# Kernel optimization log

Hardware: AMD Instinct MI355X
Metric: run time of the kernel (lower is better)

Reference implementation:

```python
import jax, jax.numpy as jnp
import numpy as np
from jax import lax

B, IN_N, MID_N, OUT_N, K, L, WH = 16, 256, 256, 256, 3, 4096, 1024
EPS = 1e-5


def att_conv(x, W, b=None):
    # x: [B, Cin, L], W: [B, Cout, Cin, K] -> per-sample conv1d, padding='same'
    pl, pr = (K - 1) // 2, K // 2
    xp = jnp.pad(x, ((0, 0), (0, 0), (pl, pr)))
    out = 0.
    for t in range(K):  # small fixed K, unrolled shifted-slice einsum
        out = out + jnp.einsum('bcl,boc->bol', lax.dynamic_slice_in_dim(xp, t, L, 2), W[..., t])
    if b is not None:
        out = out + b[:, :, None]
    return out


def batch_norm(x, w, b):
    # training-mode BN over (N, L) per channel, biased variance
    mean = x.mean((0, 2), keepdims=True)
    var = ((x - mean) ** 2).mean((0, 2), keepdims=True)
    return (x - mean) * (w[None, :, None] / jnp.sqrt(var + EPS)) + b[None, :, None]


def se_module(x, w1, b1, w2, b2):
    s = x.mean(2, keepdims=True)  # [B, C, 1]
    s = jax.nn.relu(jnp.einsum('bcl,oc->bol', s, w1) + b1[None, :, None])
    s = jax.nn.sigmoid(jnp.einsum('bcl,oc->bol', s, w2) + b2[None, :, None])
    return x * s


def setup_inputs() -> dict:
    key = jax.random.key(0)
    ks = jax.random.split(key, 16)
    f = lambda k, sh, sc=0.02: jax.random.normal(k, sh, jnp.float32) * sc
    return {
        'x': f(ks[0], (B, IN_N, L), 1.0),
        'att1': f(ks[1], (B, MID_N, WH), 1.0),
        'att2': f(ks[2], (B, MID_N, WH), 1.0),
        'att3': f(ks[3], (B, OUT_N, WH), 1.0),
        'w1_w': f(ks[4], (IN_N * K, WH)), 'w1_b': jnp.zeros((IN_N * K,), jnp.float32),
        'w2_w': f(ks[5], (MID_N * K, WH)), 'w2_b': jnp.zeros((MID_N * K,), jnp.float32),
        'w3_w': f(ks[6], (MID_N * K, WH)), 'w3_b': jnp.zeros((MID_N * K,), jnp.float32),
        'b1_w': f(ks[7], (1, WH)), 'b1_b': jnp.zeros((1,), jnp.float32),
        'bn2_w': jnp.full((MID_N,), 0.1, jnp.float32), 'bn2_b': jnp.zeros((MID_N,), jnp.float32),
        'bn3_w': jnp.full((OUT_N,), 0.1, jnp.float32), 'bn3_b': jnp.zeros((OUT_N,), jnp.float32),
        'se1_w': f(ks[8], (OUT_N, OUT_N)), 'se1_b': jnp.zeros((OUT_N,), jnp.float32),
        'se2_w': f(ks[9], (OUT_N, OUT_N)), 'se2_b': jnp.zeros((OUT_N,), jnp.float32),
    }


def reference(x, att1, att2, att3, w1_w, w1_b, w2_w, w2_b, w3_w, w3_b,
              b1_w, b1_b, bn2_w, bn2_b, bn3_w, bn3_b, se1_w, se1_b, se2_w, se2_b):
    shortcut = x  # in_n == out_n, no downsample -> Identity
    # hypernetwork weight generation (Linear on last dim)
    W1 = (att1 @ w1_w.T + w1_b).reshape(B, MID_N, IN_N, K)
    W2 = (att2 @ w2_w.T + w2_b).reshape(B, MID_N, MID_N, K)
    W3 = (att3 @ w3_w.T + w3_b).reshape(B, OUT_N, MID_N, K)
    b1 = (att1 @ b1_w.T + b1_b)[..., 0]  # [B, mid_n]
    h = jax.nn.relu(att_conv(x, W1, b1))
    h = jax.nn.relu(batch_norm(att_conv(h, W2), bn2_w, bn2_b))
    h = jax.nn.relu(batch_norm(att_conv(h, W3), bn3_w, bn3_b))
    out = jax.nn.relu(se_module(h, se1_w, se1_b, se2_w, se2_b) + shortcut)
    return out
```

## Files before the change

### kernel.cpp

```cpp
#include <hip/hip_runtime.h>
#include <hip/hip_bf16.h>

using bf16 = __hip_bfloat16;
typedef __attribute__((ext_vector_type(4))) float f32x4;
typedef __attribute__((ext_vector_type(8))) short short8;
typedef __attribute__((ext_vector_type(2))) unsigned int uint2v;
typedef __attribute__((ext_vector_type(4))) unsigned int uint4v;

#define DEVI static __device__ __forceinline__

DEVI unsigned short f2b(float f){
  unsigned int u = __float_as_uint(f);
  unsigned int r = (u + 0x7fffu + ((u >> 16) & 1u)) >> 16;
  return (unsigned short)r;
}
DEVI float b2f(unsigned short u){
  return __uint_as_float(((unsigned int)u) << 16);
}

DEVI void gload16(const void* g, void* l){
  __builtin_amdgcn_global_load_lds(
      (const __attribute__((address_space(1))) unsigned int*)g,
      (__attribute__((address_space(3))) unsigned int*)l, 16, 0, 0);
}

__global__ __launch_bounds__(256) void k_transpose_x(const float* __restrict__ x,
                                                     bf16* __restrict__ xt)
{
  __shared__ float tile[64][65];
  const int b = blockIdx.z, l0 = blockIdx.x*64, c0 = blockIdx.y*64;
  const int tid = threadIdx.x;
  {
    const int r = tid >> 2, q = tid & 3;
    const float* src = x + ((size_t)(b*256 + c0 + r))*4096 + l0 + q*16;
    #pragma unroll
    for (int j = 0; j < 4; ++j){
      const f32x4 v = *reinterpret_cast<const f32x4*>(src + j*4);
      #pragma unroll
      for (int e = 0; e < 4; ++e) tile[r][q*16 + j*4 + e] = v[e];
    }
  }
  __syncthreads();
  {
    const int jr = tid >> 2, cq = tid & 3;
    unsigned int w[8];
    #pragma unroll
    for (int e = 0; e < 8; ++e){
      const float lo = tile[cq*16 + 2*e][jr];
      const float hi = tile[cq*16 + 2*e + 1][jr];
      w[e] = (unsigned int)f2b(lo) | ((unsigned int)f2b(hi) << 16);
    }
    unsigned short* dst = (unsigned short*)xt + ((size_t)b*4098 + l0 + jr + 1)*256 + c0 + cq*16;
    uint4v a0 = {w[0],w[1],w[2],w[3]}, a1 = {w[4],w[5],w[6],w[7]};
    *reinterpret_cast<uint4v*>(dst)     = a0;
    *reinterpret_cast<uint4v*>(dst + 8) = a1;
  }
}

__global__ void k_zero_pads(bf16* __restrict__ xt, bf16* __restrict__ h1t)
{
  const int b = blockIdx.x, tid = threadIdx.x;
  const size_t top = (size_t)b*4098*256 + tid;
  const size_t bot = (size_t)b*4098*256 + (size_t)4097*256 + tid;
  unsigned short* px = (unsigned short*)xt;
  unsigned short* ph = (unsigned short*)h1t;
  px[top] = 0; px[bot] = 0; ph[top] = 0; ph[bot] = 0;
}

__global__ __launch_bounds__(256) void k_cvt3(const float* __restrict__ s0, const float* __restrict__ s1,
                                              const float* __restrict__ s2, bf16* __restrict__ dst, int n1)
{
  const size_t total = (size_t)3 * (size_t)n1 / 4;
  for (size_t i = (size_t)blockIdx.x*256 + threadIdx.x; i < total; i += (size_t)gridDim.x*256){
    const size_t e = i*4;
    const int which = (int)(e / (size_t)n1);
    const size_t off = e - (size_t)which*(size_t)n1;
    const float* s = which==0 ? s0 : which==1 ? s1 : s2;
    const f32x4 v = *reinterpret_cast<const f32x4*>(s + off);
    uint2v p;
    p[0] = (unsigned)f2b(v[0]) | ((unsigned)f2b(v[1])<<16);
    p[1] = (unsigned)f2b(v[2]) | ((unsigned)f2b(v[3])<<16);
    *reinterpret_cast<uint2v*>((unsigned short*)dst + e) = p;
  }
}


__global__ __launch_bounds__(512, 2) void k_gen(const bf16* __restrict__ attb, const bf16* __restrict__ wbp,
                                                const float* __restrict__ bias0, const float* __restrict__ bias1,
                                                const float* __restrict__ bias2, bf16* __restrict__ Wt)
{
  __shared__ bf16 sAll[4*16384];
  const int flat = blockIdx.x + (blockIdx.z << 4);
  const int xcd = flat & 7, s = flat >> 3;
  const int t = s % 3, tau = (s/3)*8 + xcd;
  const int i = tau >> 4, bo = tau & 15;
  const int bo0 = bo*256;
  const bf16* __restrict__ A  = wbp  + (size_t)i*768*1024 + (size_t)t*1024;
  const bf16* __restrict__ Bt = attb + (size_t)i*4096*1024 + (size_t)bo0*1024;
  const float* __restrict__ bias = (i==0) ? bias0 : (i==1) ? bias1 : bias2;
  const int tid = threadIdx.x, lane = tid & 63, wid = tid >> 6;
  const int wr = wid >> 2, wc = wid & 3;
  const int frow = lane & 15, g = lane >> 4;
  f32x4 acc[8][4] = {};

#define GEN_STAGE(kt, bufi) { \
    const int kc = (kt)*64; \
    _Pragma("unroll") \
    for (int j = 0; j < 4; ++j){ \
      const int slot = tid + j*512, r = slot >> 3, s7 = slot & 7; \
      const int cc = (s7 ^ (r & 7)) * 8; \
      gload16(A + (size_t)r*3072 + kc + cc, &sAll[(bufi)*16384 + slot*8]); \
    } \
    _Pragma("unroll") \
    for (int j = 0; j < 4; ++j){ \
      const int slot = tid + j*512, r = slot >> 3, s7 = slot & 7; \
      const int cc = (s7 ^ (r & 7)) * 8; \
      gload16(Bt + (size_t)r*1024 + kc + cc, &sAll[32768 + (bufi)*16384 + slot*8]); \
    } \
  }

  GEN_STAGE(0, 0);
  #pragma unroll 1
  for (int kt = 0; kt < 16; ++kt){
    const int buf = kt & 1;
    if (kt + 1 < 16){
      GEN_STAGE(kt+1, buf^1);
      asm volatile("s_waitcnt vmcnt(8)" ::: "memory");
    } else {
      asm volatile("s_waitcnt vmcnt(0)" ::: "memory");
    }
    __builtin_amdgcn_s_barrier();
    __builtin_amdgcn_sched_barrier(0);
    const bf16* pA = sAll + buf*16384;
    const bf16* pB = sAll + 32768 + buf*16384;
    #pragma unroll
    for (int ks = 0; ks < 2; ++ks){
      short8 bfr[4];
      #pragma unroll
      for (int n = 0; n < 4; ++n){
        const int row = wc*64 + n*16 + frow;
        const int sl = (ks*4 + g) ^ (row & 7);
        bfr[n] = *reinterpret_cast<const short8*>(pB + row*64 + sl*8);
      }
      __builtin_amdgcn_s_setprio(1);
      #pragma unroll
      for (int m = 0; m < 8; ++m){
        const int row = wr*128 + m*16 + frow;
        const int sl = (ks*4 + g) ^ (row & 7);
        const short8 af = *reinterpret_cast<const short8*>(pA + row*64 + sl*8);
        #pragma unroll
        for (int n = 0; n < 4; ++n)
          acc[m][n] = __builtin_amdgcn_mfma_f32_16x16x32_bf16(af, bfr[n], acc[m][n], 0, 0, 0);
      }
      __builtin_amdgcn_s_setprio(0);
    }
    __builtin_amdgcn_sched_barrier(0);
    __builtin_amdgcn_s_barrier();
    __builtin_amdgcn_sched_barrier(0);
  }
#undef GEN_STAGE

  #pragma unroll
  for (int m = 0; m < 8; ++m){
    const int col = wr*128 + m*16 + g*4;
    float bi[4];
    #pragma unroll
    for (int j = 0; j < 4; ++j) bi[j] = bias[(col + j)*3 + t];
    #pragma unroll
    for (int n = 0; n < 4; ++n){
      const int row = wc*64 + n*16 + frow;
      uint2v p;
      p[0] = (unsigned)f2b(acc[m][n][0] + bi[0]) | ((unsigned)f2b(acc[m][n][1] + bi[1]) << 16);
      p[1] = (unsigned)f2b(acc[m][n][2] + bi[2]) | ((unsigned)f2b(acc[m][n][3] + bi[3]) << 16);
      const int chunk = (col >> 3) ^ (row & 31);
      *reinterpret_cast<uint2v*>((char*)sAll + row*512 + chunk*16 + (g&1)*8) = p;
    }
  }
  __syncthreads();
  {
    char* gp = (char*)Wt + 2*(((size_t)(i*16 + bo)*3 + t)*65536);
    #pragma unroll
    for (int p2 = 0; p2 < 16; ++p2){
      const int row = p2*16 + (tid >> 5);
      const int c = tid & 31;
      const int cs2 = c ^ (row & 31);
      const uint4v v = *reinterpret_cast<const uint4v*>((const char*)sAll + row*512 + cs2*16);
      *reinterpret_cast<uint4v*>(gp + (size_t)row*512 + c*16) = v;
    }
  }
}

__global__ __launch_bounds__(256) void k_b1(const float* __restrict__ att1, const float* __restrict__ b1w,
                                            const float* __restrict__ b1b, float* __restrict__ out)
{
  const int m = blockIdx.x*4 + (threadIdx.x >> 6);
  const int lane = threadIdx.x & 63;
  const float* a = att1 + (size_t)m*1024;
  float s = 0.f;
  for (int k = lane*4; k < 1024; k += 256){
    const f32x4 v = *reinterpret_cast<const f32x4*>(a + k);
    const f32x4 w = *reinterpret_cast<const f32x4*>(b1w + k);
    s += v[0]*w[0] + v[1]*w[1] + v[2]*w[2] + v[3]*w[3];
  }
  #pragma unroll
  for (int d = 32; d > 0; d >>= 1) s += __shfl_down(s, d);
  if (lane == 0) out[m] = s + b1b[0];
}

__global__ __launch_bounds__(512, 2) void k_conv(const bf16* __restrict__ Xt, const bf16* __restrict__ W,
                                                 const float* __restrict__ bias, bf16* __restrict__ out,
                                                 int outBatchStride, int outRowOff, int applyRelu,
                                                 float* __restrict__ statSum, float* __restrict__ statSq)
{
  __shared__ bf16 sAll[4*16384];
  const int flat = blockIdx.x + (blockIdx.z << 4);
  const int xcd = flat & 7, slot = flat >> 3;
  const int b = 2*xcd + (slot >> 4);
  const int l0 = (slot & 15)*256;
  const int tid = threadIdx.x, lane = tid & 63, wid = tid >> 6;
  const int wr = wid >> 2, wc = wid & 3;
  const int frow = lane & 15, g = lane >> 4;
  f32x4 acc[8][4] = {};

#define CONV_STAGE(kt, bufi) { \
    const int ct3 = (kt)/3, tt = (kt) - ct3*3, c0 = ct3*64; \
    const bf16* Ab = W  + (((size_t)b*3 + tt)*256)*256 + c0; \
    const bf16* Bb = Xt + ((size_t)b*4098 + l0 + tt)*256 + c0; \
    _Pragma("unroll") \
    for (int j = 0; j < 4; ++j){ \
      const int slotq = tid + j*512, r = slotq >> 3, s7 = slotq & 7; \
      const int cc = (s7 ^ (r & 7)) * 8; \
      gload16(Ab + (size_t)r*256 + cc, &sAll[(bufi)*16384 + slotq*8]); \
    } \
    _Pragma("unroll") \
    for (int j = 0; j < 4; ++j){ \
      const int slotq = tid + j*512, r = slotq >> 3, s7 = slotq & 7; \
      const int cc = (s7 ^ (r & 7)) * 8; \
      gload16(Bb + (size_t)r*256 + cc, &sAll[32768 + (bufi)*16384 + slotq*8]); \
    } \
  }

  CONV_STAGE(0, 0);
  #pragma unroll 1
  for (int kt = 0; kt < 12; ++kt){
    const int buf = kt & 1;
    if (kt + 1 < 12){
      CONV_STAGE(kt+1, buf^1);
      asm volatile("s_waitcnt vmcnt(8)" ::: "memory");
    } else {
      asm volatile("s_waitcnt vmcnt(0)" ::: "memory");
    }
    __builtin_amdgcn_s_barrier();
    __builtin_amdgcn_sched_barrier(0);
    const bf16* pA = sAll + buf*16384;
    const bf16* pB = sAll + 32768 + buf*16384;
    #pragma unroll
    for (int ks = 0; ks < 2; ++ks){
      short8 bfr[4];
      #pragma unroll
      for (int n = 0; n < 4; ++n){
        const int row = wc*64 + n*16 + frow;
        const int sl = (ks*4 + g) ^ (row & 7);
        bfr[n] = *reinterpret_cast<const short8*>(pB + row*64 + sl*8);
      }
      __builtin_amdgcn_s_setprio(1);
      #pragma unroll
      for (int m = 0; m < 8; ++m){
        const int row = wr*128 + m*16 + frow;
        const int sl = (ks*4 + g) ^ (row & 7);
        const short8 af = *reinterpret_cast<const short8*>(pA + row*64 + sl*8);
        #pragma unroll
        for (int n = 0; n < 4; ++n)
          acc[m][n] = __builtin_amdgcn_mfma_f32_16x16x32_bf16(af, bfr[n], acc[m][n], 0, 0, 0);
      }
      __builtin_amdgcn_s_setprio(0);
    }
    __builtin_amdgcn_sched_barrier(0);
    __builtin_amdgcn_s_barrier();
    __builtin_amdgcn_sched_barrier(0);
  }
#undef CONV_STAGE

  float cs[8][4] = {{0.f}}, cq[8][4] = {{0.f}};
  #pragma unroll
  for (int m = 0; m < 8; ++m){
    const int col = wr*128 + m*16 + g*4;
    float bi[4] = {0.f, 0.f, 0.f, 0.f};
    if (bias){
      const f32x4 bv = *reinterpret_cast<const f32x4*>(bias + b*256 + col);
      bi[0]=bv[0]; bi[1]=bv[1]; bi[2]=bv[2]; bi[3]=bv[3];
    }
    #pragma unroll
    for (int n = 0; n < 4; ++n){
      const int row = wc*64 + n*16 + frow;
      float v[4];
      #pragma unroll
      for (int j = 0; j < 4; ++j){
        v[j] = acc[m][n][j] + bi[j];
        if (applyRelu) v[j] = fmaxf(v[j], 0.f);
        cs[m][j] += v[j];
        cq[m][j] += v[j]*v[j];
      }
      uint2v p;
      p[0] = (unsigned)f2b(v[0]) | ((unsigned)f2b(v[1]) << 16);
      p[1] = (unsigned)f2b(v[2]) | ((unsigned)f2b(v[3]) << 16);
      const int chunk = (col >> 3) ^ (row & 31);
      *reinterpret_cast<uint2v*>((char*)sAll + row*512 + chunk*16 + (g&1)*8) = p;
    }
  }
  __syncthreads();
  {
    char* gp = (char*)out + 2*((size_t)b*outBatchStride + (size_t)(l0 + outRowOff)*256);
    #pragma unroll
    for (int p2 = 0; p2 < 16; ++p2){
      const int row = p2*16 + (tid >> 5);
      const int c = tid & 31;
      const int cs2 = c ^ (row & 31);
      const uint4v v = *reinterpret_cast<const uint4v*>((const char*)sAll + row*512 + cs2*16);
      *reinterpret_cast<uint4v*>(gp + (size_t)row*512 + c*16) = v;
    }
  }
  if (statSum){
    #pragma unroll
    for (int m = 0; m < 8; ++m)
      #pragma unroll
      for (int j = 0; j < 4; ++j){
        #pragma unroll
        for (int d = 1; d < 16; d <<= 1){
          cs[m][j] += __shfl_xor(cs[m][j], d);
          cq[m][j] += __shfl_xor(cq[m][j], d);
        }
      }
    __syncthreads();
    float* ls = (float*)sAll;
    float* lq = ls + 1024;
    if (frow == 0){
      #pragma unroll
      for (int m = 0; m < 8; ++m)
        #pragma unroll
        for (int j = 0; j < 4; ++j){
          ls[wid*128 + m*16 + g*4 + j] = cs[m][j];
          lq[wid*128 + m*16 + g*4 + j] = cq[m][j];
        }
    }
    __syncthreads();
    if (tid < 256){
      const int o = tid, half = o >> 7, idx = o & 127;
      float s = 0.f, qq = 0.f;
      #pragma unroll
      for (int wv = 0; wv < 4; ++wv){
        s  += ls[(half*4 + wv)*128 + idx];
        qq += lq[(half*4 + wv)*128 + idx];
      }
      atomicAdd(statSum + o, s);
      atomicAdd(statSq  + o, qq);
    }
  }
}

__global__ void k_bnfin(const float* __restrict__ sum, const float* __restrict__ sq,
                        const float* __restrict__ g, const float* __restrict__ bb,
                        float* __restrict__ scale, float* __restrict__ shift)
{
  const int o = threadIdx.x;
  const float inv = 1.f/65536.f;
  const float m = sum[o]*inv;
  const float v = fmaxf(sq[o]*inv - m*m, 0.f);
  const float sc = g[o] / sqrtf(v + 1e-5f);
  scale[o] = sc;
  shift[o] = bb[o] - m*sc;
}

__global__ __launch_bounds__(256) void k_norm2(const bf16* __restrict__ y, const float* __restrict__ scale,
                                               const float* __restrict__ shift, bf16* __restrict__ h)
{
  const int gr = blockIdx.x*8 + (threadIdx.x >> 5);
  const int oc = threadIdx.x & 31;
  const int b = gr / 4098, lp = gr - b*4098;
  unsigned short* dst = (unsigned short*)h + (size_t)gr*256 + oc*8;
  if (lp == 0 || lp == 4097){
    uint4v z = {0u,0u,0u,0u};
    *reinterpret_cast<uint4v*>(dst) = z;
    return;
  }
  const unsigned short* src = (const unsigned short*)y + ((size_t)b*4096 + (lp-1))*256 + oc*8;
  const uint4v in = *reinterpret_cast<const uint4v*>(src);
  const f32x4 sA0 = *reinterpret_cast<const f32x4*>(scale + oc*8);
  const f32x4 sA1 = *reinterpret_cast<const f32x4*>(scale + oc*8 + 4);
  const f32x4 hA0 = *reinterpret_cast<const f32x4*>(shift + oc*8);
  const f32x4 hA1 = *reinterpret_cast<const f32x4*>(shift + oc*8 + 4);
  uint4v ov;
  #pragma unroll
  for (int e = 0; e < 4; ++e){
    const unsigned int w = in[e];
    const float sc0 = (e<2) ? sA0[2*e] : sA1[2*e-4];
    const float sc1 = (e<2) ? sA0[2*e+1] : sA1[2*e-3];
    const float sh0 = (e<2) ? hA0[2*e] : hA1[2*e-4];
    const float sh1 = (e<2) ? hA0[2*e+1] : hA1[2*e-3];
    const float v0 = fmaxf(b2f((unsigned short)(w & 0xffffu))*sc0 + sh0, 0.f);
    const float v1 = fmaxf(b2f((unsigned short)(w >> 16))*sc1 + sh1, 0.f);
    ov[e] = (unsigned)f2b(v0) | ((unsigned)f2b(v1) << 16);
  }
  *reinterpret_cast<uint4v*>(dst) = ov;
}

__global__ __launch_bounds__(256) void k_norm3(bf16* __restrict__ y, const float* __restrict__ scale,
                                               const float* __restrict__ shift, float* __restrict__ s_sum)
{
  __shared__ float red[8][256];
  const int tid = threadIdx.x;
  const int rr = tid >> 5, oc = tid & 31;
  const size_t row = (size_t)blockIdx.x*8 + rr;
  const int b = (int)(row >> 12);
  unsigned short* p = (unsigned short*)y + row*256 + oc*8;
  const uint4v in = *reinterpret_cast<const uint4v*>(p);
  const f32x4 sA0 = *reinterpret_cast<const f32x4*>(scale + oc*8);
  const f32x4 sA1 = *reinterpret_cast<const f32x4*>(scale + oc*8 + 4);
  const f32x4 hA0 = *reinterpret_cast<const f32x4*>(shift + oc*8);
  const f32x4 hA1 = *reinterpret_cast<const f32x4*>(shift + oc*8 + 4);
  uint4v ov;
  float loc[8];
  #pragma unroll
  for (int e = 0; e < 4; ++e){
    const unsigned int w = in[e];
    const float sc0 = (e<2) ? sA0[2*e] : sA1[2*e-4];
    const float sc1 = (e<2) ? sA0[2*e+1] : sA1[2*e-3];
    const float sh0 = (e<2) ? hA0[2*e] : hA1[2*e-4];
    const float sh1 = (e<2) ? hA0[2*e+1] : hA1[2*e-3];
    const float v0 = fmaxf(b2f((unsigned short)(w & 0xffffu))*sc0 + sh0, 0.f);
    const float v1 = fmaxf(b2f((unsigned short)(w >> 16))*sc1 + sh1, 0.f);
    loc[2*e] = v0; loc[2*e+1] = v1;
    ov[e] = (unsigned)f2b(v0) | ((unsigned)f2b(v1) << 16);
  }
  *reinterpret_cast<uint4v*>(p) = ov;
  #pragma unroll
  for (int j = 0; j < 8; ++j) red[rr][oc*8 + j] = loc[j];
  __syncthreads();
  const int o = tid;
  float tot = 0.f;
  #pragma unroll
  for (int r2 = 0; r2 < 8; ++r2) tot += red[r2][o];
  atomicAdd(&s_sum[(size_t)b*256 + o], tot);
}

__global__ __launch_bounds__(256) void k_se(const float* __restrict__ s_sum, const float* __restrict__ w1,
                                            const float* __restrict__ b1, const float* __restrict__ w2,
                                            const float* __restrict__ b2, float* __restrict__ s2)
{
  __shared__ float sv[256];
  __shared__ float t1[256];
  const int b = blockIdx.x, o = threadIdx.x;
  sv[o] = s_sum[(size_t)b*256 + o] * (1.f/4096.f);
  __syncthreads();
  float a = b1[o];
  for (int c = 0; c < 256; ++c) a += w1[(size_t)o*256 + c] * sv[c];
  t1[o] = fmaxf(a, 0.f);
  __syncthreads();
  float a2 = b2[o];
  for (int c = 0; c < 256; ++c) a2 += w2[(size_t)o*256 + c] * t1[c];
  s2[(size_t)b*256 + o] = 1.f / (1.f + expf(-a2));
}

__global__ __launch_bounds__(256) void k_final(const bf16* __restrict__ h3, const float* __restrict__ s2,
                                               const float* __restrict__ x, float* __restrict__ out)
{
  __shared__ float tile[64][65];
  const int b = blockIdx.z, o0 = blockIdx.y*64, l0 = blockIdx.x*64;
  const int tid = threadIdx.x;
  {
    const int r = tid >> 2, q = tid & 3;
    const unsigned short* src = (const unsigned short*)h3 + ((size_t)b*4096 + l0 + r)*256 + o0 + q*16;
    const uint4v a0 = *reinterpret_cast<const uint4v*>(src);
    const uint4v a1 = *reinterpret_cast<const uint4v*>(src + 8);
    #pragma unroll
    for (int e = 0; e < 4; ++e){
      tile[r][q*16 + 2*e]         = b2f((unsigned short)(a0[e] & 0xffffu));
      tile[r][q*16 + 2*e + 1]     = b2f((unsigned short)(a0[e] >> 16));
      tile[r][q*16 + 8 + 2*e]     = b2f((unsigned short)(a1[e] & 0xffffu));
      tile[r][q*16 + 8 + 2*e + 1] = b2f((unsigned short)(a1[e] >> 16));
    }
  }
  __syncthreads();
  {
    const int orow = tid >> 2, q = tid & 3;
    const int o = o0 + orow;
    const float sc = s2[(size_t)b*256 + o];
    const float* xs = x + ((size_t)b*256 + o)*4096 + l0 + q*16;
    float* dst = out + ((size_t)b*256 + o)*4096 + l0 + q*16;
    #pragma unroll
    for (int k = 0; k < 16; k += 4){
      const f32x4 xv = *reinterpret_cast<const f32x4*>(xs + k);
      f32x4 r;
      #pragma unroll
      for (int e = 0; e < 4; ++e)
        r[e] = fmaxf(tile[q*16 + k + e][orow]*sc + xv[e], 0.f);
      *reinterpret_cast<f32x4*>(dst + k) = r;
    }
  }
}

extern "C" void kernel_launch(void* const* d_in, const int* in_sizes, int n_in,
                              void* d_out, int out_size, void* d_ws, size_t ws_size,
                              hipStream_t stream)
{
  const float* x     = (const float*)d_in[0];
  const float* att1  = (const float*)d_in[1];
  const float* att2  = (const float*)d_in[2];
  const float* att3  = (const float*)d_in[3];
  const float* w1_w  = (const float*)d_in[4];
  const float* w1_b  = (const float*)d_in[5];
  const float* w2_w  = (const float*)d_in[6];
  const float* w2_b  = (const float*)d_in[7];
  const float* w3_w  = (const float*)d_in[8];
  const float* w3_b  = (const float*)d_in[9];
  const float* b1_w  = (const float*)d_in[10];
  const float* b1_b  = (const float*)d_in[11];
  const float* bn2_w = (const float*)d_in[12];
  const float* bn2_b = (const float*)d_in[13];
  const float* bn3_w = (const float*)d_in[14];
  const float* bn3_b = (const float*)d_in[15];
  const float* se1_w = (const float*)d_in[16];
  const float* se1_b = (const float*)d_in[17];
  const float* se2_w = (const float*)d_in[18];
  const float* se2_b = (const float*)d_in[19];

  char* ws = (char*)d_ws;
  bf16*  xT   = (bf16*)(ws + 0);
  bf16*  h1T  = (bf16*)(ws + 33570816);
  bf16*  y2T  = (bf16*)(ws + 67141632);
  bf16*  h2T  = (bf16*)(ws + 100696064);
  bf16*  Wt   = (bf16*)(ws + 134266880);
  bf16*  attb = (bf16*)(ws + 153141248);
  bf16*  wb   = (bf16*)(ws + 178307072);
  float* b1v  = (float*)(ws + 183025664);
  float* st   = (float*)(ws + 183042048);
  float* bn2sum = st;
  float* bn2sq  = st + 256;
  float* bn3sum = st + 512;
  float* bn3sq  = st + 768;
  float* s_sum  = st + 1024;
  float* scale2 = st + 5120;
  float* shift2 = st + 5376;
  float* scale3 = st + 5632;
  float* shift3 = st + 5888;
  float* s2v    = st + 6144;
  bf16*  y3T  = (bf16*)(ws + 0);

  hipMemsetAsync(st, 0, 5120*sizeof(float), stream);

  k_transpose_x<<<dim3(64,4,16),256,0,stream>>>(x, xT);
  k_zero_pads<<<16,256,0,stream>>>(xT, h1T);
  k_cvt3<<<2048,256,0,stream>>>(att1, att2, att3, attb, 4096*1024);
  k_cvt3<<<512,256,0,stream>>>(w1_w, w2_w, w3_w, wb, 768*1024);
  k_gen<<<dim3(16,1,9),512,0,stream>>>(attb, wb, w1_b, w2_b, w3_b, Wt);
  k_b1<<<1024,256,0,stream>>>(att1, b1_w, b1_b, b1v);

  k_conv<<<dim3(16,1,16),512,0,stream>>>(xT,  Wt,                           b1v,     h1T, 4098*256, 1, 1, nullptr, nullptr);
  k_conv<<<dim3(16,1,16),512,0,stream>>>(h1T, Wt + (size_t)1*16*3*256*256,  nullptr, y2T, 4096*256, 0, 0, bn2sum, bn2sq);
  k_bnfin<<<1,256,0,stream>>>(bn2sum, bn2sq, bn2_w, bn2_b, scale2, shift2);
  k_norm2<<<8196,256,0,stream>>>(y2T, scale2, shift2, h2T);
  k_conv<<<dim3(16,1,16),512,0,stream>>>(h2T, Wt + (size_t)2*16*3*256*256,  nullptr, y3T, 4096*256, 0, 0, bn3sum, bn3sq);
  k_bnfin<<<1,256,0,stream>>>(bn3sum, bn3sq, bn3_w, bn3_b, scale3, shift3);
  k_norm3<<<8192,256,0,stream>>>(y3T, scale3, shift3, s_sum);
  k_se<<<16,256,0,stream>>>(s_sum, se1_w, se1_b, se2_w, se2_b, s2v);
  k_final<<<dim3(64,4,16),256,0,stream>>>((const bf16*)y3T, s2v, x, (float*)d_out);
}
```

Measured before the change: 309.2 us.

## Fuse att fp32-to-bf16 conversion into hypernet GEMM and shrink conv tiles

The hypernetwork GEMM now loads fp32 attention rows straight from global memory into registers, converts them to bf16 and writes them to LDS itself. This removes the separate conversion kernel and its bf16 round trip through memory. The K step is halved to 32 to fit the smaller LDS budget, and the epilogue is split into two passes. The conv kernel now uses 256x128 tiles with a K step of 32, twice as many blocks and launch bounds of 4 blocks per CU, to raise occupancy. The trade is more barriers per unit of K and less reuse per tile.

```diff
diff --git a/kernel.cpp b/kernel.cpp
--- a/kernel.cpp
+++ b/kernel.cpp
@@ -84,109 +84,134 @@
   }
 }
 
-
-__global__ __launch_bounds__(512, 2) void k_gen(const bf16* __restrict__ attb, const bf16* __restrict__ wbp,
+__global__ __launch_bounds__(512, 2) void k_gen(const float* __restrict__ att1f, const float* __restrict__ att2f,
+                                                const float* __restrict__ att3f, const bf16* __restrict__ wbp,
                                                 const float* __restrict__ bias0, const float* __restrict__ bias1,
                                                 const float* __restrict__ bias2, bf16* __restrict__ Wt)
 {
-  __shared__ bf16 sAll[4*16384];
+  __shared__ bf16 sAll[32768];
   const int flat = blockIdx.x + (blockIdx.z << 4);
   const int xcd = flat & 7, s = flat >> 3;
   const int t = s % 3, tau = (s/3)*8 + xcd;
   const int i = tau >> 4, bo = tau & 15;
   const int bo0 = bo*256;
-  const bf16* __restrict__ A  = wbp  + (size_t)i*768*1024 + (size_t)t*1024;
-  const bf16* __restrict__ Bt = attb + (size_t)i*4096*1024 + (size_t)bo0*1024;
+  const bf16*  __restrict__ A  = wbp + (size_t)i*768*1024 + (size_t)t*1024;
+  const float* __restrict__ Bf = ((i==0) ? att1f : (i==1) ? att2f : att3f) + (size_t)bo0*1024;
   const float* __restrict__ bias = (i==0) ? bias0 : (i==1) ? bias1 : bias2;
   const int tid = threadIdx.x, lane = tid & 63, wid = tid >> 6;
   const int wr = wid >> 2, wc = wid & 3;
   const int frow = lane & 15, g = lane >> 4;
   f32x4 acc[8][4] = {};
-
-#define GEN_STAGE(kt, bufi) { \
-    const int kc = (kt)*64; \
+  f32x4 rN[4];
+
+  const int rB = tid >> 1, hB = tid & 1;
+  const float* bsBase = Bf + (size_t)rB*1024 + hB*16;
+
+#define GEN_STAGE_A(kt, bufi) { \
     _Pragma("unroll") \
-    for (int j = 0; j < 4; ++j){ \
-      const int slot = tid + j*512, r = slot >> 3, s7 = slot & 7; \
-      const int cc = (s7 ^ (r & 7)) * 8; \
-      gload16(A + (size_t)r*3072 + kc + cc, &sAll[(bufi)*16384 + slot*8]); \
-    } \
-    _Pragma("unroll") \
-    for (int j = 0; j < 4; ++j){ \
-      const int slot = tid + j*512, r = slot >> 3, s7 = slot & 7; \
-      const int cc = (s7 ^ (r & 7)) * 8; \
-      gload16(Bt + (size_t)r*1024 + kc + cc, &sAll[32768 + (bufi)*16384 + slot*8]); \
-    } \
-  }
-
-  GEN_STAGE(0, 0);
+    for (int j = 0; j < 2; ++j){ \
+      const int q = tid + j*512, r = q >> 2, s3 = q & 3; \
+      const int cc = (s3 ^ ((r >> 1) & 3)) * 8; \
+      gload16(A + (size_t)r*3072 + (kt)*32 + cc, &sAll[(bufi)*8192 + q*8]); \
+    } }
+
+#define GEN_WRITE_B(bufi) { \
+    unsigned short* wp = (unsigned short*)&sAll[16384 + (bufi)*8192]; \
+    uint4v w0, w1; \
+    w0[0] = (unsigned)f2b(rN[0][0]) | ((unsigned)f2b(rN[0][1])<<16); \
+    w0[1] = (unsigned)f2b(rN[0][2]) | ((unsigned)f2b(rN[0][3])<<16); \
+    w0[2] = (unsigned)f2b(rN[1][0]) | ((unsigned)f2b(rN[1][1])<<16); \
+    w0[3] = (unsigned)f2b(rN[1][2]) | ((unsigned)f2b(rN[1][3])<<16); \
+    w1[0] = (unsigned)f2b(rN[2][0]) | ((unsigned)f2b(rN[2][1])<<16); \
+    w1[1] = (unsigned)f2b(rN[2][2]) | ((unsigned)f2b(rN[2][3])<<16); \
+    w1[2] = (unsigned)f2b(rN[3][0]) | ((unsigned)f2b(rN[3][1])<<16); \
+    w1[3] = (unsigned)f2b(rN[3][2]) | ((unsigned)f2b(rN[3][3])<<16); \
+    const int sl0 = (hB*2 + 0) ^ ((rB >> 1) & 3); \
+    const int sl1 = (hB*2 + 1) ^ ((rB >> 1) & 3); \
+    *reinterpret_cast<uint4v*>(wp + rB*32 + sl0*8) = w0; \
+    *reinterpret_cast<uint4v*>(wp + rB*32 + sl1*8) = w1; }
+
+  #pragma unroll
+  for (int q = 0; q < 4; ++q) rN[q] = *reinterpret_cast<const f32x4*>(bsBase + q*4);
+  GEN_STAGE_A(0, 0);
+  asm volatile("s_waitcnt vmcnt(0)" ::: "memory");
+  GEN_WRITE_B(0);
+  asm volatile("s_waitcnt lgkmcnt(0)" ::: "memory");
+  __builtin_amdgcn_s_barrier();
+
   #pragma unroll 1
-  for (int kt = 0; kt < 16; ++kt){
-    const int buf = kt & 1;
-    if (kt + 1 < 16){
-      GEN_STAGE(kt+1, buf^1);
-      asm volatile("s_waitcnt vmcnt(8)" ::: "memory");
+  for (int kt = 0; kt < 32; ++kt){
+    const int p = kt & 1;
+    if (kt + 1 < 32){
+      #pragma unroll
+      for (int q = 0; q < 4; ++q) rN[q] = *reinterpret_cast<const f32x4*>(bsBase + (kt+1)*32 + q*4);
+      GEN_STAGE_A(kt+1, p^1);
+      asm volatile("s_waitcnt vmcnt(6)" ::: "memory");
     } else {
       asm volatile("s_waitcnt vmcnt(0)" ::: "memory");
     }
     __builtin_amdgcn_s_barrier();
-    __builtin_amdgcn_sched_barrier(0);
-    const bf16* pA = sAll + buf*16384;
-    const bf16* pB = sAll + 32768 + buf*16384;
-    #pragma unroll
-    for (int ks = 0; ks < 2; ++ks){
-      short8 bfr[4];
-      #pragma unroll
-      for (int n = 0; n < 4; ++n){
-        const int row = wc*64 + n*16 + frow;
-        const int sl = (ks*4 + g) ^ (row & 7);
-        bfr[n] = *reinterpret_cast<const short8*>(pB + row*64 + sl*8);
-      }
-      __builtin_amdgcn_s_setprio(1);
-      #pragma unroll
-      for (int m = 0; m < 8; ++m){
-        const int row = wr*128 + m*16 + frow;
-        const int sl = (ks*4 + g) ^ (row & 7);
-        const short8 af = *reinterpret_cast<const short8*>(pA + row*64 + sl*8);
-        #pragma unroll
-        for (int n = 0; n < 4; ++n)
-          acc[m][n] = __builtin_amdgcn_mfma_f32_16x16x32_bf16(af, bfr[n], acc[m][n], 0, 0, 0);
-      }
-      __builtin_amdgcn_s_setprio(0);
-    }
-    __builtin_amdgcn_sched_barrier(0);
-    __builtin_amdgcn_s_barrier();
-    __builtin_amdgcn_sched_barrier(0);
-  }
-#undef GEN_STAGE
-
-  #pragma unroll
-  for (int m = 0; m < 8; ++m){
-    const int col = wr*128 + m*16 + g*4;
-    float bi[4];
-    #pragma unroll
-    for (int j = 0; j < 4; ++j) bi[j] = bias[(col + j)*3 + t];
+    const bf16* pA = sAll + p*8192;
+    const bf16* pB = sAll + 16384 + p*8192;
+    short8 bfr[4];
     #pragma unroll
     for (int n = 0; n < 4; ++n){
       const int row = wc*64 + n*16 + frow;
-      uint2v p;
-      p[0] = (unsigned)f2b(acc[m][n][0] + bi[0]) | ((unsigned)f2b(acc[m][n][1] + bi[1]) << 16);
-      p[1] = (unsigned)f2b(acc[m][n][2] + bi[2]) | ((unsigned)f2b(acc[m][n][3] + bi[3]) << 16);
-      const int chunk = (col >> 3) ^ (row & 31);
-      *reinterpret_cast<uint2v*>((char*)sAll + row*512 + chunk*16 + (g&1)*8) = p;
-    }
-  }
-  __syncthreads();
-  {
-    char* gp = (char*)Wt + 2*(((size_t)(i*16 + bo)*3 + t)*65536);
-    #pragma unroll
-    for (int p2 = 0; p2 < 16; ++p2){
-      const int row = p2*16 + (tid >> 5);
+      const int sl = g ^ ((row >> 1) & 3);
+      bfr[n] = *reinterpret_cast<const short8*>(pB + row*32 + sl*8);
+    }
+    __builtin_amdgcn_s_setprio(1);
+    #pragma unroll
+    for (int m = 0; m < 8; ++m){
+      const int row = wr*128 + m*16 + frow;
+      const int sl = g ^ ((row >> 1) & 3);
+      const short8 af = *reinterpret_cast<const short8*>(pA + row*32 + sl*8);
+      #pragma unroll
+      for (int n = 0; n < 4; ++n)
+        acc[m][n] = __builtin_amdgcn_mfma_f32_16x16x32_bf16(af, bfr[n], acc[m][n], 0, 0, 0);
+    }
+    __builtin_amdgcn_s_setprio(0);
+    if (kt + 1 < 32){
+      GEN_WRITE_B(p^1);
+    }
+    asm volatile("s_waitcnt lgkmcnt(0)" ::: "memory");
+    __builtin_amdgcn_s_barrier();
+  }
+#undef GEN_STAGE_A
+#undef GEN_WRITE_B
+
+  char* gp = (char*)Wt + 2*(((size_t)(i*16 + bo)*3 + t)*65536);
+  #pragma unroll
+  for (int pass = 0; pass < 2; ++pass){
+    if ((wc >> 1) == pass){
+      #pragma unroll
+      for (int m = 0; m < 8; ++m){
+        const int col = wr*128 + m*16 + g*4;
+        float bi[4];
+        #pragma unroll
+        for (int j = 0; j < 4; ++j) bi[j] = bias[(col + j)*3 + t];
+        #pragma unroll
+        for (int n = 0; n < 4; ++n){
+          const int row = wc*64 + n*16 + frow;
+          const int lrow = row & 127;
+          uint2v pk;
+          pk[0] = (unsigned)f2b(acc[m][n][0] + bi[0]) | ((unsigned)f2b(acc[m][n][1] + bi[1]) << 16);
+          pk[1] = (unsigned)f2b(acc[m][n][2] + bi[2]) | ((unsigned)f2b(acc[m][n][3] + bi[3]) << 16);
+          const int chunk = (col >> 3) ^ (lrow & 31);
+          *reinterpret_cast<uint2v*>((char*)sAll + lrow*512 + chunk*16 + (g&1)*8) = pk;
+        }
+      }
+    }
+    __syncthreads();
+    #pragma unroll
+    for (int it = 0; it < 8; ++it){
+      const int lrow = it*16 + (tid >> 5);
       const int c = tid & 31;
-      const int cs2 = c ^ (row & 31);
-      const uint4v v = *reinterpret_cast<const uint4v*>((const char*)sAll + row*512 + cs2*16);
-      *reinterpret_cast<uint4v*>(gp + (size_t)row*512 + c*16) = v;
-    }
+      const int cs2 = c ^ (lrow & 31);
+      const uint4v v = *reinterpret_cast<const uint4v*>((const char*)sAll + lrow*512 + cs2*16);
+      *reinterpret_cast<uint4v*>(gp + (size_t)(pass*128 + lrow)*512 + c*16) = v;
+    }
+    __syncthreads();
   }
 }
 
@@ -207,84 +232,77 @@
   if (lane == 0) out[m] = s + b1b[0];
 }
 
-__global__ __launch_bounds__(512, 2) void k_conv(const bf16* __restrict__ Xt, const bf16* __restrict__ W,
+__global__ __launch_bounds__(512, 4) void k_conv(const bf16* __restrict__ Xt, const bf16* __restrict__ W,
                                                  const float* __restrict__ bias, bf16* __restrict__ out,
                                                  int outBatchStride, int outRowOff, int applyRelu,
                                                  float* __restrict__ statSum, float* __restrict__ statSq)
 {
-  __shared__ bf16 sAll[4*16384];
-  const int flat = blockIdx.x + (blockIdx.z << 4);
+  __shared__ bf16 sAll[32768];
+  const int flat = blockIdx.x + (blockIdx.z << 5);
   const int xcd = flat & 7, slot = flat >> 3;
-  const int b = 2*xcd + (slot >> 4);
-  const int l0 = (slot & 15)*256;
+  const int b = 2*xcd + (slot >> 5);
+  const int l0 = (slot & 31) * 128;
   const int tid = threadIdx.x, lane = tid & 63, wid = tid >> 6;
-  const int wr = wid >> 2, wc = wid & 3;
+  const int wr = wid >> 1, wc = wid & 1;
   const int frow = lane & 15, g = lane >> 4;
-  f32x4 acc[8][4] = {};
+  f32x4 acc[4][4] = {};
 
 #define CONV_STAGE(kt, bufi) { \
-    const int ct3 = (kt)/3, tt = (kt) - ct3*3, c0 = ct3*64; \
+    const int ct3 = (kt)/3, tt = (kt) - ct3*3, c0 = ct3*32; \
     const bf16* Ab = W  + (((size_t)b*3 + tt)*256)*256 + c0; \
     const bf16* Bb = Xt + ((size_t)b*4098 + l0 + tt)*256 + c0; \
     _Pragma("unroll") \
-    for (int j = 0; j < 4; ++j){ \
-      const int slotq = tid + j*512, r = slotq >> 3, s7 = slotq & 7; \
-      const int cc = (s7 ^ (r & 7)) * 8; \
-      gload16(Ab + (size_t)r*256 + cc, &sAll[(bufi)*16384 + slotq*8]); \
+    for (int j = 0; j < 2; ++j){ \
+      const int q = tid + j*512, r = q >> 2, s3 = q & 3; \
+      const int cc = (s3 ^ ((r >> 1) & 3)) * 8; \
+      gload16(Ab + (size_t)r*256 + cc, &sAll[(bufi)*8192 + q*8]); \
     } \
-    _Pragma("unroll") \
-    for (int j = 0; j < 4; ++j){ \
-      const int slotq = tid + j*512, r = slotq >> 3, s7 = slotq & 7; \
-      const int cc = (s7 ^ (r & 7)) * 8; \
-      gload16(Bb + (size_t)r*256 + cc, &sAll[32768 + (bufi)*16384 + slotq*8]); \
-    } \
+    { const int q = tid, r = q >> 2, s3 = q & 3; \
+      const int cc = (s3 ^ ((r >> 1) & 3)) * 8; \
+      gload16(Bb + (size_t)r*256 + cc, &sAll[16384 + (bufi)*4096 + q*8]); } \
   }
 
   CONV_STAGE(0, 0);
   #pragma unroll 1
-  for (int kt = 0; kt < 12; ++kt){
+  for (int kt = 0; kt < 24; ++kt){
     const int buf = kt & 1;
-    if (kt + 1 < 12){
+    if (kt + 1 < 24){
       CONV_STAGE(kt+1, buf^1);
-      asm volatile("s_waitcnt vmcnt(8)" ::: "memory");
+      asm volatile("s_waitcnt vmcnt(3)" ::: "memory");
     } else {
       asm volatile("s_waitcnt vmcnt(0)" ::: "memory");
     }
     __builtin_amdgcn_s_barrier();
-    __builtin_amdgcn_sched_barrier(0);
-    const bf16* pA = sAll + buf*16384;
-    const bf16* pB = sAll + 32768 + buf*16384;
-    #pragma unroll
-    for (int ks = 0; ks < 2; ++ks){
-      short8 bfr[4];
-      #pragma unroll
-      for (int n = 0; n < 4; ++n){
-        const int row = wc*64 + n*16 + frow;
-        const int sl = (ks*4 + g) ^ (row & 7);
-        bfr[n] = *reinterpret_cast<const short8*>(pB + row*64 + sl*8);
-      }
-      __builtin_amdgcn_s_setprio(1);
-      #pragma unroll
-      for (int m = 0; m < 8; ++m){
-        const int row = wr*128 + m*16 + frow;
-        const int sl = (ks*4 + g) ^ (row & 7);
-        const short8 af = *reinterpret_cast<const short8*>(pA + row*64 + sl*8);
-        #pragma unroll
-        for (int n = 0; n < 4; ++n)
-          acc[m][n] = __builtin_amdgcn_mfma_f32_16x16x32_bf16(af, bfr[n], acc[m][n], 0, 0, 0);
-      }
-      __builtin_amdgcn_s_setprio(0);
-    }
-    __builtin_amdgcn_sched_barrier(0);
+    const bf16* pA = sAll + buf*8192;
+    const bf16* pB = sAll + 16384 + buf*4096;
+    short8 bfr[4], afr[4];
+    #pragma unroll
+    for (int n = 0; n < 4; ++n){
+      const int row = wc*64 + n*16 + frow;
+      const int sl = g ^ ((row >> 1) & 3);
+      bfr[n] = *reinterpret_cast<const short8*>(pB + row*32 + sl*8);
+    }
+    #pragma unroll
+    for (int m = 0; m < 4; ++m){
+      const int row = wr*64 + m*16 + frow;
+      const int sl = g ^ ((row >> 1) & 3);
+      afr[m] = *reinterpret_cast<const short8*>(pA + row*32 + sl*8);
+    }
+    __builtin_amdgcn_s_setprio(1);
+    #pragma unroll
+    for (int m = 0; m < 4; ++m)
+      #pragma unroll
+      for (int n = 0; n < 4; ++n)
+        acc[m][n] = __builtin_amdgcn_mfma_f32_16x16x32_bf16(afr[m], bfr[n], acc[m][n], 0, 0, 0);
+    __builtin_amdgcn_s_setprio(0);
     __builtin_amdgcn_s_barrier();
-    __builtin_amdgcn_sched_barrier(0);
   }
 #undef CONV_STAGE
 
-  float cs[8][4] = {{0.f}}, cq[8][4] = {{0.f}};
-  #pragma unroll
-  for (int m = 0; m < 8; ++m){
-    const int col = wr*128 + m*16 + g*4;
+  float cs[4][4] = {{0.f}}, cq[4][4] = {{0.f}};
+  #pragma unroll
+  for (int m = 0; m < 4; ++m){
+    const int col = wr*64 + m*16 + g*4;
     float bi[4] = {0.f, 0.f, 0.f, 0.f};
     if (bias){
       const f32x4 bv = *reinterpret_cast<const f32x4*>(bias + b*256 + col);
@@ -301,19 +319,19 @@
         cs[m][j] += v[j];
         cq[m][j] += v[j]*v[j];
       }
-      uint2v p;
-      p[0] = (unsigned)f2b(v[0]) | ((unsigned)f2b(v[1]) << 16);
-      p[1] = (unsigned)f2b(v[2]) | ((unsigned)f2b(v[3]) << 16);
+      uint2v pk;
+      pk[0] = (unsigned)f2b(v[0]) | ((unsigned)f2b(v[1]) << 16);
+      pk[1] = (unsigned)f2b(v[2]) | ((unsigned)f2b(v[3]) << 16);
       const int chunk = (col >> 3) ^ (row & 31);
-      *reinterpret_cast<uint2v*>((char*)sAll + row*512 + chunk*16 + (g&1)*8) = p;
+      *reinterpret_cast<uint2v*>((char*)sAll + row*512 + chunk*16 + (g&1)*8) = pk;
     }
   }
   __syncthreads();
   {
     char* gp = (char*)out + 2*((size_t)b*outBatchStride + (size_t)(l0 + outRowOff)*256);
     #pragma unroll
-    for (int p2 = 0; p2 < 16; ++p2){
-      const int row = p2*16 + (tid >> 5);
+    for (int it = 0; it < 8; ++it){
+      const int row = it*16 + (tid >> 5);
       const int c = tid & 31;
       const int cs2 = c ^ (row & 31);
       const uint4v v = *reinterpret_cast<const uint4v*>((const char*)sAll + row*512 + cs2*16);
@@ -322,7 +340,7 @@
   }
   if (statSum){
     #pragma unroll
-    for (int m = 0; m < 8; ++m)
+    for (int m = 0; m < 4; ++m)
       #pragma unroll
       for (int j = 0; j < 4; ++j){
         #pragma unroll
@@ -333,25 +351,21 @@
       }
     __syncthreads();
     float* ls = (float*)sAll;
-    float* lq = ls + 1024;
+    float* lq = ls + 512;
     if (frow == 0){
       #pragma unroll
-      for (int m = 0; m < 8; ++m)
+      for (int m = 0; m < 4; ++m)
         #pragma unroll
         for (int j = 0; j < 4; ++j){
-          ls[wid*128 + m*16 + g*4 + j] = cs[m][j];
-          lq[wid*128 + m*16 + g*4 + j] = cq[m][j];
+          ls[wid*64 + m*16 + g*4 + j] = cs[m][j];
+          lq[wid*64 + m*16 + g*4 + j] = cq[m][j];
         }
     }
     __syncthreads();
     if (tid < 256){
-      const int o = tid, half = o >> 7, idx = o & 127;
-      float s = 0.f, qq = 0.f;
-      #pragma unroll
-      for (int wv = 0; wv < 4; ++wv){
-        s  += ls[(half*4 + wv)*128 + idx];
-        qq += lq[(half*4 + wv)*128 + idx];
-      }
+      const int o = tid, wrI = o >> 6, idx = o & 63;
+      const float s  = ls[(wrI*2 + 0)*64 + idx] + ls[(wrI*2 + 1)*64 + idx];
+      const float qq = lq[(wrI*2 + 0)*64 + idx] + lq[(wrI*2 + 1)*64 + idx];
       atomicAdd(statSum + o, s);
       atomicAdd(statSq  + o, qq);
     }
@@ -530,7 +544,6 @@
   bf16*  y2T  = (bf16*)(ws + 67141632);
   bf16*  h2T  = (bf16*)(ws + 100696064);
   bf16*  Wt   = (bf16*)(ws + 134266880);
-  bf16*  attb = (bf16*)(ws + 153141248);
   bf16*  wb   = (bf16*)(ws + 178307072);
   float* b1v  = (float*)(ws + 183025664);
   float* st   = (float*)(ws + 183042048);
@@ -550,16 +563,15 @@
 
   k_transpose_x<<<dim3(64,4,16),256,0,stream>>>(x, xT);
   k_zero_pads<<<16,256,0,stream>>>(xT, h1T);
-  k_cvt3<<<2048,256,0,stream>>>(att1, att2, att3, attb, 4096*1024);
   k_cvt3<<<512,256,0,stream>>>(w1_w, w2_w, w3_w, wb, 768*1024);
-  k_gen<<<dim3(16,1,9),512,0,stream>>>(attb, wb, w1_b, w2_b, w3_b, Wt);
+  k_gen<<<dim3(16,1,9),512,0,stream>>>(att1, att2, att3, wb, w1_b, w2_b, w3_b, Wt);
   k_b1<<<1024,256,0,stream>>>(att1, b1_w, b1_b, b1v);
 
-  k_conv<<<dim3(16,1,16),512,0,stream>>>(xT,  Wt,                           b1v,     h1T, 4098*256, 1, 1, nullptr, nullptr);
-  k_conv<<<dim3(16,1,16),512,0,stream>>>(h1T, Wt + (size_t)1*16*3*256*256,  nullptr, y2T, 4096*256, 0, 0, bn2sum, bn2sq);
+  k_conv<<<dim3(32,1,16),512,0,stream>>>(xT,  Wt,                           b1v,     h1T, 4098*256, 1, 1, nullptr, nullptr);
+  k_conv<<<dim3(32,1,16),512,0,stream>>>(h1T, Wt + (size_t)1*16*3*256*256,  nullptr, y2T, 4096*256, 0, 0, bn2sum, bn2sq);
   k_bnfin<<<1,256,0,stream>>>(bn2sum, bn2sq, bn2_w, bn2_b, scale2, shift2);
   k_norm2<<<8196,256,0,stream>>>(y2T, scale2, shift2, h2T);
-  k_conv<<<dim3(16,1,16),512,0,stream>>>(h2T, Wt + (size_t)2*16*3*256*256,  nullptr, y3T, 4096*256, 0, 0, bn3sum, bn3sq);
+  k_conv<<<dim3(32,1,16),512,0,stream>>>(h2T, Wt + (size_t)2*16*3*256*256,  nullptr, y3T, 4096*256, 0, 0, bn3sum, bn3sq);
   k_bnfin<<<1,256,0,stream>>>(bn3sum, bn3sq, bn3_w, bn3_b, scale3, shift3);
   k_norm3<<<8192,256,0,stream>>>(y3T, scale3, shift3, s_sum);
   k_se<<<16,256,0,stream>>>(s_sum, se1_w, se1_b, se2_w, se2_b, s2v);
```

Measured after the change: 327.9 us. +6.0%, slower.
